# Optimization experiments

Measured on AMD Instinct MI355X. Metric: run time of the kernel, lower is better.

The kernel has to match this reference:

```python
import jax, jax.numpy as jnp
import numpy as np
import itertools

N_PARTICLES = 8388608
GRID_RES = 2048
BOX_SIZE = 1000.0

def _rotations_47():
    perms = list(itertools.permutations([0, 1, 2]))
    signs = list(itertools.product([1, -1], repeat=3))
    mats = []
    for s in signs:
        for p in perms:
            M = np.zeros((3, 3), np.float32)
            M[0, p[0]] = s[0]; M[1, p[1]] = s[1]; M[2, p[2]] = s[2]
            mats.append(M)
    return jnp.asarray(np.stack(mats)[1:])  # drop identity -> 47 matrices

# Analytic stand-ins for jax_cosmo background quantities (EdS-like forms).
def _Gp(a):
    return a ** 1.5

def _dGfa(a):
    return 1.5 * jnp.sqrt(a)

def _a_of_chi(chi):
    return 1.0 / (1.0 + chi / 3000.0)

def _paint_2d(pos, center, width, box_size, res):
    """CIC scatter of particles inside a z-slab onto a [res,res] density plane."""
    z = pos[:, 2]
    sel = ((z >= center - width * 0.5) & (z < center + width * 0.5)).astype(pos.dtype)
    xy = pos[:, :2] * (res / box_size)          # grid coordinates, [N,2]
    i0 = jnp.floor(xy)
    f = xy - i0                                  # CIC fractional offsets
    i0 = i0.astype(jnp.int32)
    ix0 = jnp.mod(i0[:, 0], res); iy0 = jnp.mod(i0[:, 1], res)
    ix1 = jnp.mod(i0[:, 0] + 1, res); iy1 = jnp.mod(i0[:, 1] + 1, res)
    fx, fy = f[:, 0], f[:, 1]
    flat = jnp.zeros((res * res,), dtype=pos.dtype)
    flat = flat.at[ix0 * res + iy0].add(sel * (1 - fx) * (1 - fy))
    flat = flat.at[ix1 * res + iy0].add(sel * fx * (1 - fy))
    flat = flat.at[ix0 * res + iy1].add(sel * (1 - fx) * fy)
    flat = flat.at[ix1 * res + iy1].add(sel * fx * fy)
    return flat.reshape(res, res)

def setup_inputs():
    key = jax.random.key(0)
    k1, k2 = jax.random.split(key)
    positions = jax.random.uniform(k1, (N_PARTICLES, 3), jnp.float32) * BOX_SIZE
    velocities = jax.random.normal(k2, (N_PARTICLES, 3), jnp.float32) * 2.0
    return {
        "positions": positions,
        "velocities": velocities,
        "rotations": _rotations_47(),
        "observer": jnp.zeros((3,), jnp.float32),
        "r_centers": jnp.asarray([250.0, 750.0, 1250.0, 1750.0], jnp.float32),
        "density_widths": jnp.full((4,), 500.0, jnp.float32),
        "t": jnp.float32(0.8),
        "max_comoving_distance": jnp.float32(BOX_SIZE),
        "box_size": jnp.float32(BOX_SIZE),
        "shell_idx": 2,
        "rotation_idx": 1,
        "grid_res": GRID_RES,
    }

def reference(positions, velocities, rotations, observer, r_centers, density_widths,
              t, max_comoving_distance, box_size, shell_idx, rotation_idx, grid_res):
    r_center = r_centers[shell_idx]
    width = density_widths[shell_idx]
    inside_box = r_center + width * 0.5 <= max_comoving_distance

    def inside_branch(args):
        pos, _vel = args
        return _paint_2d(pos, r_center, width, box_size, grid_res)

    def telephoto_branch(args):
        pos, vel = args
        M = rotations[rotation_idx % 47]                                   # [3,3]
        shift = jnp.floor(r_center / max_comoving_distance) * max_comoving_distance
        p_rot = (pos - observer) @ M.T                                      # rotate about observer
        z_axis = jnp.array([0.0, 0.0, 1.0], pos.dtype)
        p_shift = p_rot + z_axis * shift
        v_rot = vel @ M.T
        dist = jnp.linalg.norm(p_shift - observer, axis=-1)                 # [N]
        a_tgt = _a_of_chi(dist)[:, None]                                    # per-particle target scale factor
        ac = jnp.sqrt(t * a_tgt)
        drift = (_Gp(a_tgt) - _Gp(t)) / _dGfa(ac)
        p_drift = p_shift + drift * v_rot
        return _paint_2d(p_drift + observer, r_center, width, box_size, grid_res)

    return jax.lax.cond(inside_box, inside_branch, telephoto_branch, (positions, velocities))
```

## Files before the change

kernel.cpp:

```cpp
#include <hip/hip_runtime.h>
#include <cmath>


#define TSZ    128
#define NBKT   256
#define CAPB   2
#define SLOTS  (CAPB*16)
#define DEPTH  26
#define NTH    256
#define NBLK   960
#define VEC    4
#define NSUB   3
#define DESCMAX 256
#define SENT   0xFFFFFFFFu

__device__ __forceinline__ float fast_rcp(float x)  { return __builtin_amdgcn_rcpf(x); }
__device__ __forceinline__ float fast_sqrt(float x) { return __builtin_amdgcn_sqrtf(x); }

__device__ __forceinline__ int wrap_idx(int v, int res) {
    v += (v < 0) ? res : 0;
    v += (v < 0) ? res : 0;
    v += (v < 0) ? res : 0;
    v -= (v >= res) ? res : 0;
    v -= (v >= res) ? res : 0;
    v -= (v >= res) ? res : 0;
    if (v < 0 || v >= res) { v %= res; if (v < 0) v += res; }
    return v;
}

__device__ __forceinline__ void scatter_direct(float* __restrict__ out, int res,
                                               int gx0, int gy0, float fx, float fy) {
    int gx1 = gx0 + 1; if (gx1 >= res) gx1 = 0;
    int gy1 = gy0 + 1; if (gy1 >= res) gy1 = 0;
    atomicAdd(&out[gx0 * res + gy0], (1.0f - fx) * (1.0f - fy));
    atomicAdd(&out[gx1 * res + gy0], fx * (1.0f - fy));
    atomicAdd(&out[gx0 * res + gy1], (1.0f - fx) * fy);
    atomicAdd(&out[gx1 * res + gy1], fx * fy);
}

__device__ __forceinline__ void rec_decode(unsigned rec, int b, int tiles,
                                           int& gx, int& gy, float& fx, float& fy) {
    int tx = b / tiles, ty = b - tx * tiles;
    gx = (tx << 7) + (int)(rec >> 25);
    gy = (ty << 7) + (int)((rec >> 18) & 127u);
    fx = (float)((rec >> 9) & 511u) * (1.0f / 512.0f);
    fy = (float)(rec & 511u) * (1.0f / 512.0f);
}

struct Uni {
    float m00, m01, m02, m10, m11, m12, m20, m21, m22;
    float ox, oy, oz, shift;
    float r_lo, r_hi, t, gp_t, scale;
    int   resm1, res, tiles;
    bool  inside;
};

struct PR {
    unsigned rec, st;
    int ix0, iy0;
    float fx, fy;
    bool val;
};

__device__ __forceinline__ PR tp_compute(
    const Uni& u, unsigned dummy,
    float px, float py, float pz, float vx, float vy, float vz)
{
    float X, Y, Z;
    if (u.inside) {
        X = px; Y = py; Z = pz;
    } else {
        const float qx_ = px - u.ox, qy_ = py - u.oy, qz_ = pz - u.oz;
        float rx = u.m00 * qx_ + u.m01 * qy_ + u.m02 * qz_;
        float ry = u.m10 * qx_ + u.m11 * qy_ + u.m12 * qz_;
        float rz = u.m20 * qx_ + u.m21 * qy_ + u.m22 * qz_ + u.shift;

        const float vrx = u.m00 * vx + u.m01 * vy + u.m02 * vz;
        const float vry = u.m10 * vx + u.m11 * vy + u.m12 * vz;
        const float vrz = u.m20 * vx + u.m21 * vy + u.m22 * vz;

        const float dx = rx - u.ox, dy = ry - u.oy, dz = rz - u.oz;
        const float dist  = fast_sqrt(dx * dx + dy * dy + dz * dz);
        const float a_tgt = fast_rcp(1.0f + dist * (1.0f / 3000.0f));
        const float ac    = fast_sqrt(u.t * a_tgt);
        const float gp_a  = a_tgt * fast_sqrt(a_tgt);
        const float drift = (gp_a - u.gp_t) * fast_rcp(1.5f * fast_sqrt(ac));

        X = rx + drift * vrx + u.ox;
        Y = ry + drift * vry + u.oy;
        Z = rz + drift * vrz + u.oz;
    }
    PR o;
    o.val = (Z >= u.r_lo && Z < u.r_hi);

    const float gx = X * u.scale, gy = Y * u.scale;
    const float fgx = floorf(gx), fgy = floorf(gy);
    o.fx = gx - fgx; o.fy = gy - fgy;
    o.ix0 = ((int)fgx) & u.resm1;
    o.iy0 = ((int)fgy) & u.resm1;
    const unsigned st = (unsigned)((o.ix0 >> 7) * u.tiles + (o.iy0 >> 7));
    o.st = o.val ? st : dummy;

    unsigned qx = (unsigned)(o.fx * 512.0f + 0.5f); if (qx > 511u) qx = 511u;
    unsigned qy = (unsigned)(o.fy * 512.0f + 0.5f); if (qy > 511u) qy = 511u;
    o.rec = ((unsigned)(o.ix0 & 127) << 25) | ((unsigned)(o.iy0 & 127) << 18)
          | (qx << 9) | qy;
    return o;
}

__device__ __forceinline__ void tp_finish(
    const Uni& u, const PR& o, unsigned p,
    unsigned* __restrict__ fill, unsigned* __restrict__ buf,
    float* __restrict__ out)
{
    if (!o.val) return;
    if (p < DEPTH) buf[o.st * DEPTH + p] = o.rec;
    else { atomicSub(&fill[o.st], 1u); scatter_direct(out, u.res, o.ix0, o.iy0, o.fx, o.fy); }
}

__device__ __forceinline__ void tp_process(
    const Uni& u, float px, float py, float pz, float vx, float vy, float vz,
    unsigned* __restrict__ fill, unsigned* __restrict__ buf,
    float* __restrict__ out)
{
    const PR o = tp_compute(u, 0u, px, py, pz, vx, vy, vz);
    if (!o.val) return;
    unsigned p = atomicAdd(&fill[o.st], 1u);
    tp_finish(u, o, p, fill, buf, out);
}

__global__ __launch_bounds__(NTH) void tp_bin(
    const float* __restrict__ pos, const float* __restrict__ vel,
    const float* __restrict__ rotations, const float* __restrict__ observer,
    const float* __restrict__ r_centers, const float* __restrict__ widths,
    const float* __restrict__ t_p, const float* __restrict__ maxd_p,
    const float* __restrict__ box_p, const int* __restrict__ shell_p,
    const int* __restrict__ ridx_p,
    unsigned char* __restrict__ cnts, unsigned* __restrict__ grec,
    float* __restrict__ out, int res, int tiles, int n, int rounds)
{
    __shared__ unsigned fill[NBKT + 64];
    __shared__ unsigned buf[NBKT * DEPTH];
    __shared__ unsigned descB[DESCMAX];
    __shared__ unsigned descD[DESCMAX];
    __shared__ unsigned char cidA[NBKT];
    __shared__ unsigned ndesc;

    const int tid = threadIdx.x;
    for (int b = tid; b < NBKT + 64; b += NTH) fill[b] = 0;
    if (tid < NBKT) cidA[tid] = 0;
    if (tid == 0) ndesc = 0;

    Uni u;
    {
        const int   shell    = shell_p[0];
        const float r_center = r_centers[shell];
        const float width    = widths[shell];
        const float maxd     = maxd_p[0];
        const float box      = box_p[0];
        u.t      = t_p[0];
        u.inside = (r_center + width * 0.5f) <= maxd;
        int ridx = ridx_p[0] % 47; if (ridx < 0) ridx += 47;
        const float* M = rotations + 9 * ridx;
        u.m00 = M[0]; u.m01 = M[1]; u.m02 = M[2];
        u.m10 = M[3]; u.m11 = M[4]; u.m12 = M[5];
        u.m20 = M[6]; u.m21 = M[7]; u.m22 = M[8];
        u.ox = observer[0]; u.oy = observer[1]; u.oz = observer[2];
        u.shift = floorf(r_center / maxd) * maxd;
        u.r_lo = r_center - width * 0.5f;
        u.r_hi = r_center + width * 0.5f;
        u.gp_t = u.t * sqrtf(u.t);
        u.scale = (float)res / box;
        u.resm1 = res - 1; u.res = res; u.tiles = tiles;
    }

    const unsigned dummy = (unsigned)(NBKT + (tid & 63));
    const float4* __restrict__ pos4 = (const float4*)pos;
    const float4* __restrict__ vel4 = (const float4*)vel;

    __syncthreads();

    for (int r = 0; r < rounds; ++r) {
        #pragma unroll 1
        for (int s = 0; s < NSUB; ++s) {
            const int rc = r * NSUB + s;
            const int base = ((rc * NBLK + blockIdx.x) * NTH + tid) * VEC;
            if (base + VEC <= n) {
                const int q = base * 3 / 4;
                const float4 a = pos4[q], b = pos4[q + 1], c = pos4[q + 2];
                PR r0, r1, r2, r3;
                if (u.inside) {
                    r0 = tp_compute(u, dummy, a.x, a.y, a.z, 0, 0, 0);
                    r1 = tp_compute(u, dummy, a.w, b.x, b.y, 0, 0, 0);
                    r2 = tp_compute(u, dummy, b.z, b.w, c.x, 0, 0, 0);
                    r3 = tp_compute(u, dummy, c.y, c.z, c.w, 0, 0, 0);
                } else {
                    const float4 d = vel4[q], e = vel4[q + 1], f = vel4[q + 2];
                    r0 = tp_compute(u, dummy, a.x, a.y, a.z, d.x, d.y, d.z);
                    r1 = tp_compute(u, dummy, a.w, b.x, b.y, d.w, e.x, e.y);
                    r2 = tp_compute(u, dummy, b.z, b.w, c.x, e.z, e.w, f.x);
                    r3 = tp_compute(u, dummy, c.y, c.z, c.w, f.y, f.z, f.w);
                }
                const unsigned p0 = atomicAdd(&fill[r0.st], 1u);
                const unsigned p1 = atomicAdd(&fill[r1.st], 1u);
                const unsigned p2 = atomicAdd(&fill[r2.st], 1u);
                const unsigned p3 = atomicAdd(&fill[r3.st], 1u);
                tp_finish(u, r0, p0, fill, buf, out);
                tp_finish(u, r1, p1, fill, buf, out);
                tp_finish(u, r2, p2, fill, buf, out);
                tp_finish(u, r3, p3, fill, buf, out);
            } else {
                for (int p = 0; p < VEC; ++p) {
                    const int i = base + p;
                    if (i >= 0 && i < n)
                        tp_process(u, pos[3 * i], pos[3 * i + 1], pos[3 * i + 2],
                                   vel[3 * i], vel[3 * i + 1], vel[3 * i + 2],
                                   fill, buf, out);
                }
            }
        }
        __syncthreads();
        if (tid < NBKT) {
            const unsigned c = fill[tid];
            const unsigned k = c >> 4;
            if (k) {
                unsigned d = atomicAdd(&ndesc, k);
                unsigned cid = cidA[tid];
                for (unsigned g = 0; g < k; ++g) {
                    descB[d + g] = (unsigned)tid | ((g * 16u) << 16);
                    descD[d + g] = (cid < CAPB)
                        ? (unsigned)(((unsigned)tid * NBLK + blockIdx.x) * SLOTS + cid * 16u)
                        : SENT;
                    ++cid;
                }
                cidA[tid] = (unsigned char)cid;
            }
        }
        __syncthreads();
        const unsigned nd = ndesc;
        for (unsigned did = (unsigned)(tid >> 4); did < nd; did += NTH / 16) {
            const unsigned e = descB[did];
            const unsigned b = e & 0xffffu, so = e >> 16;
            const unsigned rv = buf[b * DEPTH + so + (tid & 15)];
            const unsigned dstb = descD[did];
            if (dstb != SENT) {
                grec[(size_t)dstb + (tid & 15)] = rv;
            } else {
                int gx0, gy0; float ffx, ffy;
                rec_decode(rv, (int)b, u.tiles, gx0, gy0, ffx, ffy);
                scatter_direct(out, u.res, gx0, gy0, ffx, ffy);
            }
        }
        __syncthreads();
        if (tid < NBKT) {
            const unsigned c = fill[tid];
            const unsigned k = c >> 4;
            if (k) {
                const unsigned resid = c - 16u * k;
                for (unsigned j = 0; j < resid; ++j)
                    buf[tid * DEPTH + j] = buf[tid * DEPTH + 16u * k + j];
                fill[tid] = resid;
            }
        }
        if (tid == 0) ndesc = 0;
        __syncthreads();
    }

    if (tid < NBKT) {
        const unsigned c = fill[tid];
        const unsigned cid = cidA[tid];
        const unsigned wc = (cid < CAPB) ? cid : (unsigned)CAPB;
        const bool rw = (c > 0) && (cid < CAPB);
        cnts[(size_t)blockIdx.x * NBKT + tid] = (unsigned char)(16u * wc + (rw ? c : 0u));
        if (c) {
            unsigned d = atomicAdd(&ndesc, 1u);
            descB[d] = (unsigned)tid | (c << 16);
            descD[d] = rw
                ? (unsigned)(((unsigned)tid * NBLK + blockIdx.x) * SLOTS + cid * 16u)
                : SENT;
        }
    }
    __syncthreads();
    const unsigned nd = ndesc;
    for (unsigned did = (unsigned)(tid >> 4); did < nd; did += NTH / 16) {
        const unsigned e = descB[did];
        const unsigned b = e & 0xffffu, c = e >> 16;
        const unsigned lane = (unsigned)(tid & 15);
        if (lane < c) {
            const unsigned rv = buf[b * DEPTH + lane];
            const unsigned dstb = descD[did];
            if (dstb != SENT) {
                grec[(size_t)dstb + lane] = rv;
            } else {
                int gx0, gy0; float ffx, ffy;
                rec_decode(rv, (int)b, u.tiles, gx0, gy0, ffx, ffy);
                scatter_direct(out, u.res, gx0, gy0, ffx, ffy);
            }
        }
    }
}

__global__ __launch_bounds__(1024) void tp_paint(
    const unsigned char* __restrict__ cnts, const unsigned* __restrict__ grec,
    float* __restrict__ out, int res, int tiles)
{
    __shared__ unsigned long long quad[4][64 * 64];
    __shared__ unsigned char cs[NBLK];
    const int b = blockIdx.x;
    const int tx = b / tiles, ty = b - tx * tiles;

    for (int c = threadIdx.x; c < 4 * 64 * 64; c += blockDim.x)
        quad[c >> 12][c & 4095] = 0ull;
    for (int i = threadIdx.x; i < NBLK; i += blockDim.x)
        cs[i] = cnts[(size_t)i * NBKT + b];
    __syncthreads();

    const unsigned* __restrict__ rr = grec + (size_t)b * NBLK * SLOTS;
    const int total = NBLK * SLOTS;
    for (int idx = threadIdx.x; idx < total; idx += blockDim.x) {
        const unsigned p = rr[idx];
        if ((idx & (SLOTS - 1)) < (int)cs[idx >> 5]) {
            const int li = (int)(p >> 25);
            const int lj = (int)((p >> 18) & 127u);
            const unsigned qx = (p >> 9) & 511u;
            const unsigned qy = p & 511u;
            const unsigned ax = 512u - qx, ay = 512u - qy;
            const unsigned long long w00 = (ax * ay + 128u) >> 8;
            const unsigned long long w01 = (ax * qy + 128u) >> 8;
            const unsigned long long w10 = (qx * ay + 128u) >> 8;
            const unsigned long long w11 = (qx * qy + 128u) >> 8;
            const unsigned long long pk = w00 | (w01 << 16) | (w10 << 32) | (w11 << 48);
            const int g = ((li & 1) << 1) | (lj & 1);
            atomicAdd(&quad[g][(li >> 1) * 64 + (lj >> 1)], pk);
        }
    }
    __syncthreads();

    for (int c = threadIdx.x; c < (TSZ + 1) * (TSZ + 1); c += blockDim.x) {
        const int i = c / (TSZ + 1), j = c - i * (TSZ + 1);
        unsigned acc = 0;
        #pragma unroll
        for (int r = 0; r < 2; ++r) {
            const int ii = i - r;
            if (ii < 0 || ii > TSZ - 1) continue;
            #pragma unroll
            for (int s = 0; s < 2; ++s) {
                const int jj = j - s;
                if (jj < 0 || jj > TSZ - 1) continue;
                const int g = ((ii & 1) << 1) | (jj & 1);
                const unsigned long long v = quad[g][(ii >> 1) * 64 + (jj >> 1)];
                acc += (unsigned)((v >> (16 * (r * 2 + s))) & 0xffffull);
            }
        }
        const float val = (float)acc * (1.0f / 1024.0f);
        int gx = tx * TSZ + i; if (gx >= res) gx -= res;
        int gy = ty * TSZ + j; if (gy >= res) gy -= res;
        float* dst = &out[gx * res + gy];
        if (i == 0 || j == 0 || i == TSZ || j == TSZ) {
            if (val != 0.0f) atomicAdd(dst, val);
        } else {
            *dst += val;
        }
    }
}

__global__ __launch_bounds__(256) void tp_direct(
    const float* __restrict__ pos, const float* __restrict__ vel,
    const float* __restrict__ rotations, const float* __restrict__ observer,
    const float* __restrict__ r_centers, const float* __restrict__ widths,
    const float* __restrict__ t_p, const float* __restrict__ maxd_p,
    const float* __restrict__ box_p, const int* __restrict__ shell_p,
    const int* __restrict__ ridx_p, float* __restrict__ out, int res, int n)
{
    int i = blockIdx.x * blockDim.x + threadIdx.x;
    if (i >= n) return;
    const int   shell    = shell_p[0];
    const float r_center = r_centers[shell];
    const float width    = widths[shell];
    const float maxd     = maxd_p[0];
    const float box      = box_p[0];
    const float t        = t_p[0];
    const bool  inside   = (r_center + width * 0.5f) <= maxd;
    int ridx = ridx_p[0] % 47; if (ridx < 0) ridx += 47;

    float px = pos[3 * i], py = pos[3 * i + 1], pz = pos[3 * i + 2];
    float X, Y, Z;
    if (inside) {
        X = px; Y = py; Z = pz;
    } else {
        const float* M = rotations + 9 * ridx;
        const float ox = observer[0], oy = observer[1], oz = observer[2];
        const float qx = px - ox, qy = py - oy, qz = pz - oz;
        float rx = M[0] * qx + M[1] * qy + M[2] * qz;
        float ry = M[3] * qx + M[4] * qy + M[5] * qz;
        float rz = M[6] * qx + M[7] * qy + M[8] * qz + floorf(r_center / maxd) * maxd;
        const float vx = vel[3 * i], vy = vel[3 * i + 1], vz = vel[3 * i + 2];
        const float vrx = M[0] * vx + M[1] * vy + M[2] * vz;
        const float vry = M[3] * vx + M[4] * vy + M[5] * vz;
        const float vrz = M[6] * vx + M[7] * vy + M[8] * vz;
        const float dx = rx - ox, dy = ry - oy, dz = rz - oz;
        const float dist  = sqrtf(dx * dx + dy * dy + dz * dz);
        const float a_tgt = 1.0f / (1.0f + dist / 3000.0f);
        const float ac    = sqrtf(t * a_tgt);
        const float drift = (a_tgt * sqrtf(a_tgt) - t * sqrtf(t)) / (1.5f * sqrtf(ac));
        X = rx + drift * vrx + ox;
        Y = ry + drift * vry + oy;
        Z = rz + drift * vrz + oz;
    }
    if (!(Z >= r_center - width * 0.5f && Z < r_center + width * 0.5f)) return;

    const float scale = (float)res / box;
    const float gx = X * scale, gy = Y * scale;
    const float fgx = floorf(gx), fgy = floorf(gy);
    scatter_direct(out, res, wrap_idx((int)fgx, res), wrap_idx((int)fgy, res),
                   gx - fgx, gy - fgy);
}

extern "C" void kernel_launch(void* const* d_in, const int* in_sizes, int n_in,
                              void* d_out, int out_size, void* d_ws, size_t ws_size,
                              hipStream_t stream) {
    const float* pos   = (const float*)d_in[0];
    const float* velv  = (const float*)d_in[1];
    const float* rot   = (const float*)d_in[2];
    const float* obs   = (const float*)d_in[3];
    const float* rc    = (const float*)d_in[4];
    const float* dw    = (const float*)d_in[5];
    const float* t     = (const float*)d_in[6];
    const float* maxd  = (const float*)d_in[7];
    const float* box   = (const float*)d_in[8];
    const int*   shell = (const int*)d_in[9];
    const int*   ridx  = (const int*)d_in[10];
    float* out = (float*)d_out;

    const int n   = in_sizes[0] / 3;
    const int res = (int)llround(sqrt((double)out_size));

    hipMemsetAsync(out, 0, (size_t)out_size * sizeof(float), stream);

    const int tiles = res / TSZ;
    const int nt2 = tiles * tiles;
    const size_t rec_bytes = (size_t)NBKT * NBLK * SLOTS * sizeof(unsigned);
    const size_t cnt_bytes = (size_t)NBLK * NBKT;
    const bool pow2 = res > 0 && (res & (res - 1)) == 0;

    if (!pow2 || res % TSZ != 0 || nt2 > NBKT ||
        (long long)res * res != (long long)out_size ||
        ws_size < rec_bytes + cnt_bytes) {
        tp_direct<<<(n + 255) / 256, 256, 0, stream>>>(
            pos, velv, rot, obs, rc, dw, t, maxd, box, shell, ridx, out, res, n);
        return;
    }

    unsigned* grec = (unsigned*)d_ws;
    unsigned char* cnts = (unsigned char*)d_ws + rec_bytes;

    const int per_round = NBLK * NTH * VEC * NSUB;
    const int rounds = (n + per_round - 1) / per_round;
    tp_bin<<<NBLK, NTH, 0, stream>>>(
        pos, velv, rot, obs, rc, dw, t, maxd, box, shell, ridx,
        cnts, grec, out, res, tiles, n, rounds);

    tp_paint<<<nt2, 1024, 0, stream>>>(cnts, grec, out, res, tiles);
}
```

Before: 295.3 us.

## Make binning wave-private with eager per-bucket flushes instead of block-wide rounds

The binning kernel now gives each wavefront its own shared-memory fill counters, bucket buffers and chunk ids. When a bucket reaches 16 records, the lane that took slot 15 flushes it at once, instead of the block running barrier-separated rounds with a descriptor list. This removes the __syncthreads and descriptor bookkeeping per round. The cost is that a single lane flushes each bucket serially with copies and residual shifts, each wave gets only one global chunk per bucket before falling back to direct atomic scatter, and the paint kernel now scans a record array indexed per wave.

Result: faster. 289.2 us (-2.1%).

```diff
diff --git a/kernel.cpp b/kernel.cpp
--- a/kernel.cpp
+++ b/kernel.cpp
@@ -4,15 +4,13 @@
 
 #define TSZ    128
 #define NBKT   256
-#define CAPB   2
-#define SLOTS  (CAPB*16)
-#define DEPTH  26
+#define DEPTH  18
+#define SLOTS  16
 #define NTH    256
-#define NBLK   960
+#define WPB    4
+#define NBLK   480
+#define NWAVES (NBLK*WPB)
 #define VEC    4
-#define NSUB   3
-#define DESCMAX 256
-#define SENT   0xFFFFFFFFu
 
 __device__ __forceinline__ float fast_rcp(float x)  { return __builtin_amdgcn_rcpf(x); }
 __device__ __forceinline__ float fast_sqrt(float x) { return __builtin_amdgcn_sqrtf(x); }
@@ -118,15 +116,40 @@
     else { atomicSub(&fill[o.st], 1u); scatter_direct(out, u.res, o.ix0, o.iy0, o.fx, o.fy); }
 }
 
-__device__ __forceinline__ void tp_process(
-    const Uni& u, float px, float py, float pz, float vx, float vy, float vz,
+__device__ __forceinline__ void flush_if(
+    const Uni& u, const PR& o, unsigned p, unsigned w,
     unsigned* __restrict__ fill, unsigned* __restrict__ buf,
-    float* __restrict__ out)
-{
-    const PR o = tp_compute(u, 0u, px, py, pz, vx, vy, vz);
-    if (!o.val) return;
-    unsigned p = atomicAdd(&fill[o.st], 1u);
-    tp_finish(u, o, p, fill, buf, out);
+    unsigned char* __restrict__ cid,
+    unsigned* __restrict__ grec, float* __restrict__ out)
+{
+    if (o.val && p == 15u) {
+        const unsigned b = o.st;
+        const unsigned c = fill[b];
+        const unsigned ci = cid[b];
+        if (ci == 0u) {
+            const size_t dst = ((size_t)b * NWAVES + w) * SLOTS;
+            #pragma unroll
+            for (int i = 0; i < 16; i += 4) {
+                uint4 v;
+                v.x = buf[b * DEPTH + i];
+                v.y = buf[b * DEPTH + i + 1];
+                v.z = buf[b * DEPTH + i + 2];
+                v.w = buf[b * DEPTH + i + 3];
+                *(uint4*)(grec + dst + i) = v;
+            }
+        } else {
+            for (int i = 0; i < 16; ++i) {
+                int gx0, gy0; float ffx, ffy;
+                rec_decode(buf[b * DEPTH + i], (int)b, u.tiles, gx0, gy0, ffx, ffy);
+                scatter_direct(out, u.res, gx0, gy0, ffx, ffy);
+            }
+        }
+        cid[b] = (unsigned char)(ci + 1u);
+        const unsigned resid = c - 16u;
+        for (unsigned j = 0; j < resid; ++j)
+            buf[b * DEPTH + j] = buf[b * DEPTH + 16u + j];
+        fill[b] = resid;
+    }
 }
 
 __global__ __launch_bounds__(NTH) void tp_bin(
@@ -137,19 +160,21 @@
     const float* __restrict__ box_p, const int* __restrict__ shell_p,
     const int* __restrict__ ridx_p,
     unsigned char* __restrict__ cnts, unsigned* __restrict__ grec,
-    float* __restrict__ out, int res, int tiles, int n, int rounds)
-{
-    __shared__ unsigned fill[NBKT + 64];
-    __shared__ unsigned buf[NBKT * DEPTH];
-    __shared__ unsigned descB[DESCMAX];
-    __shared__ unsigned descD[DESCMAX];
-    __shared__ unsigned char cidA[NBKT];
-    __shared__ unsigned ndesc;
-
-    const int tid = threadIdx.x;
-    for (int b = tid; b < NBKT + 64; b += NTH) fill[b] = 0;
-    if (tid < NBKT) cidA[tid] = 0;
-    if (tid == 0) ndesc = 0;
+    float* __restrict__ out, int res, int tiles, int n, int cpw)
+{
+    __shared__ unsigned fillS[WPB][NBKT + 64];
+    __shared__ unsigned bufS[WPB][NBKT * DEPTH];
+    __shared__ unsigned char cidS[WPB][NBKT];
+
+    const int tid  = threadIdx.x;
+    const int wv   = tid >> 6;
+    const int lane = tid & 63;
+    unsigned* __restrict__ fill = fillS[wv];
+    unsigned* __restrict__ buf  = bufS[wv];
+    unsigned char* __restrict__ cid = cidS[wv];
+
+    for (int b = lane; b < NBKT + 64; b += 64) fill[b] = 0;
+    for (int b = lane; b < NBKT; b += 64) cid[b] = 0;
 
     Uni u;
     {
@@ -174,129 +199,74 @@
         u.resm1 = res - 1; u.res = res; u.tiles = tiles;
     }
 
-    const unsigned dummy = (unsigned)(NBKT + (tid & 63));
+    const unsigned w = (unsigned)(blockIdx.x * WPB + wv);
+    const unsigned dummy = (unsigned)(NBKT + lane);
     const float4* __restrict__ pos4 = (const float4*)pos;
     const float4* __restrict__ vel4 = (const float4*)vel;
 
-    __syncthreads();
-
-    for (int r = 0; r < rounds; ++r) {
-        #pragma unroll 1
-        for (int s = 0; s < NSUB; ++s) {
-            const int rc = r * NSUB + s;
-            const int base = ((rc * NBLK + blockIdx.x) * NTH + tid) * VEC;
-            if (base + VEC <= n) {
-                const int q = base * 3 / 4;
-                const float4 a = pos4[q], b = pos4[q + 1], c = pos4[q + 2];
-                PR r0, r1, r2, r3;
-                if (u.inside) {
-                    r0 = tp_compute(u, dummy, a.x, a.y, a.z, 0, 0, 0);
-                    r1 = tp_compute(u, dummy, a.w, b.x, b.y, 0, 0, 0);
-                    r2 = tp_compute(u, dummy, b.z, b.w, c.x, 0, 0, 0);
-                    r3 = tp_compute(u, dummy, c.y, c.z, c.w, 0, 0, 0);
-                } else {
-                    const float4 d = vel4[q], e = vel4[q + 1], f = vel4[q + 2];
-                    r0 = tp_compute(u, dummy, a.x, a.y, a.z, d.x, d.y, d.z);
-                    r1 = tp_compute(u, dummy, a.w, b.x, b.y, d.w, e.x, e.y);
-                    r2 = tp_compute(u, dummy, b.z, b.w, c.x, e.z, e.w, f.x);
-                    r3 = tp_compute(u, dummy, c.y, c.z, c.w, f.y, f.z, f.w);
+    for (int k = 0; k < cpw; ++k) {
+        const int base = (((k * NWAVES + (int)w) * 64) + lane) * VEC;
+        PR pr[4];
+        if (base + VEC <= n) {
+            const int q = base * 3 / 4;
+            const float4 a = pos4[q], b = pos4[q + 1], c = pos4[q + 2];
+            if (u.inside) {
+                pr[0] = tp_compute(u, dummy, a.x, a.y, a.z, 0, 0, 0);
+                pr[1] = tp_compute(u, dummy, a.w, b.x, b.y, 0, 0, 0);
+                pr[2] = tp_compute(u, dummy, b.z, b.w, c.x, 0, 0, 0);
+                pr[3] = tp_compute(u, dummy, c.y, c.z, c.w, 0, 0, 0);
+            } else {
+                const float4 d = vel4[q], e = vel4[q + 1], f = vel4[q + 2];
+                pr[0] = tp_compute(u, dummy, a.x, a.y, a.z, d.x, d.y, d.z);
+                pr[1] = tp_compute(u, dummy, a.w, b.x, b.y, d.w, e.x, e.y);
+                pr[2] = tp_compute(u, dummy, b.z, b.w, c.x, e.z, e.w, f.x);
+                pr[3] = tp_compute(u, dummy, c.y, c.z, c.w, f.y, f.z, f.w);
+            }
+        } else {
+            #pragma unroll
+            for (int j = 0; j < VEC; ++j) {
+                const int i = base + j;
+                const bool ok = (i >= 0) && (i < n);
+                float px = 0, py = 0, pz = 0, vx = 0, vy = 0, vz = 0;
+                if (ok) {
+                    px = pos[3 * i]; py = pos[3 * i + 1]; pz = pos[3 * i + 2];
+                    if (!u.inside) {
+                        vx = vel[3 * i]; vy = vel[3 * i + 1]; vz = vel[3 * i + 2];
+                    }
                 }
-                const unsigned p0 = atomicAdd(&fill[r0.st], 1u);
-                const unsigned p1 = atomicAdd(&fill[r1.st], 1u);
-                const unsigned p2 = atomicAdd(&fill[r2.st], 1u);
-                const unsigned p3 = atomicAdd(&fill[r3.st], 1u);
-                tp_finish(u, r0, p0, fill, buf, out);
-                tp_finish(u, r1, p1, fill, buf, out);
-                tp_finish(u, r2, p2, fill, buf, out);
-                tp_finish(u, r3, p3, fill, buf, out);
-            } else {
-                for (int p = 0; p < VEC; ++p) {
-                    const int i = base + p;
-                    if (i >= 0 && i < n)
-                        tp_process(u, pos[3 * i], pos[3 * i + 1], pos[3 * i + 2],
-                                   vel[3 * i], vel[3 * i + 1], vel[3 * i + 2],
-                                   fill, buf, out);
-                }
-            }
-        }
-        __syncthreads();
-        if (tid < NBKT) {
-            const unsigned c = fill[tid];
-            const unsigned k = c >> 4;
-            if (k) {
-                unsigned d = atomicAdd(&ndesc, k);
-                unsigned cid = cidA[tid];
-                for (unsigned g = 0; g < k; ++g) {
-                    descB[d + g] = (unsigned)tid | ((g * 16u) << 16);
-                    descD[d + g] = (cid < CAPB)
-                        ? (unsigned)(((unsigned)tid * NBLK + blockIdx.x) * SLOTS + cid * 16u)
-                        : SENT;
-                    ++cid;
-                }
-                cidA[tid] = (unsigned char)cid;
-            }
-        }
-        __syncthreads();
-        const unsigned nd = ndesc;
-        for (unsigned did = (unsigned)(tid >> 4); did < nd; did += NTH / 16) {
-            const unsigned e = descB[did];
-            const unsigned b = e & 0xffffu, so = e >> 16;
-            const unsigned rv = buf[b * DEPTH + so + (tid & 15)];
-            const unsigned dstb = descD[did];
-            if (dstb != SENT) {
-                grec[(size_t)dstb + (tid & 15)] = rv;
-            } else {
+                PR t = tp_compute(u, dummy, px, py, pz, vx, vy, vz);
+                if (!ok) { t.val = false; t.st = dummy; }
+                pr[j] = t;
+            }
+        }
+        unsigned pp[4];
+        #pragma unroll
+        for (int j = 0; j < 4; ++j) pp[j] = atomicAdd(&fill[pr[j].st], 1u);
+        #pragma unroll
+        for (int j = 0; j < 4; ++j) tp_finish(u, pr[j], pp[j], fill, buf, out);
+        #pragma unroll
+        for (int j = 0; j < 4; ++j) flush_if(u, pr[j], pp[j], w, fill, buf, cid, grec, out);
+    }
+
+    #pragma unroll
+    for (int j = 0; j < NBKT / 64; ++j) {
+        const int b = lane + j * 64;
+        const unsigned c = fill[b];
+        const unsigned ci = cid[b];
+        unsigned char cb;
+        if (ci == 0u) {
+            cb = (unsigned char)c;
+            const size_t dst = ((size_t)b * NWAVES + w) * SLOTS;
+            for (unsigned i = 0; i < c; ++i) grec[dst + i] = buf[b * DEPTH + i];
+        } else {
+            cb = (unsigned char)SLOTS;
+            for (unsigned i = 0; i < c; ++i) {
                 int gx0, gy0; float ffx, ffy;
-                rec_decode(rv, (int)b, u.tiles, gx0, gy0, ffx, ffy);
+                rec_decode(buf[b * DEPTH + i], b, u.tiles, gx0, gy0, ffx, ffy);
                 scatter_direct(out, u.res, gx0, gy0, ffx, ffy);
             }
         }
-        __syncthreads();
-        if (tid < NBKT) {
-            const unsigned c = fill[tid];
-            const unsigned k = c >> 4;
-            if (k) {
-                const unsigned resid = c - 16u * k;
-                for (unsigned j = 0; j < resid; ++j)
-                    buf[tid * DEPTH + j] = buf[tid * DEPTH + 16u * k + j];
-                fill[tid] = resid;
-            }
-        }
-        if (tid == 0) ndesc = 0;
-        __syncthreads();
-    }
-
-    if (tid < NBKT) {
-        const unsigned c = fill[tid];
-        const unsigned cid = cidA[tid];
-        const unsigned wc = (cid < CAPB) ? cid : (unsigned)CAPB;
-        const bool rw = (c > 0) && (cid < CAPB);
-        cnts[(size_t)blockIdx.x * NBKT + tid] = (unsigned char)(16u * wc + (rw ? c : 0u));
-        if (c) {
-            unsigned d = atomicAdd(&ndesc, 1u);
-            descB[d] = (unsigned)tid | (c << 16);
-            descD[d] = rw
-                ? (unsigned)(((unsigned)tid * NBLK + blockIdx.x) * SLOTS + cid * 16u)
-                : SENT;
-        }
-    }
-    __syncthreads();
-    const unsigned nd = ndesc;
-    for (unsigned did = (unsigned)(tid >> 4); did < nd; did += NTH / 16) {
-        const unsigned e = descB[did];
-        const unsigned b = e & 0xffffu, c = e >> 16;
-        const unsigned lane = (unsigned)(tid & 15);
-        if (lane < c) {
-            const unsigned rv = buf[b * DEPTH + lane];
-            const unsigned dstb = descD[did];
-            if (dstb != SENT) {
-                grec[(size_t)dstb + lane] = rv;
-            } else {
-                int gx0, gy0; float ffx, ffy;
-                rec_decode(rv, (int)b, u.tiles, gx0, gy0, ffx, ffy);
-                scatter_direct(out, u.res, gx0, gy0, ffx, ffy);
-            }
-        }
+        cnts[(size_t)w * NBKT + b] = cb;
     }
 }
 
@@ -305,21 +275,21 @@
     float* __restrict__ out, int res, int tiles)
 {
     __shared__ unsigned long long quad[4][64 * 64];
-    __shared__ unsigned char cs[NBLK];
+    __shared__ unsigned char cs[NWAVES];
     const int b = blockIdx.x;
     const int tx = b / tiles, ty = b - tx * tiles;
 
     for (int c = threadIdx.x; c < 4 * 64 * 64; c += blockDim.x)
         quad[c >> 12][c & 4095] = 0ull;
-    for (int i = threadIdx.x; i < NBLK; i += blockDim.x)
+    for (int i = threadIdx.x; i < NWAVES; i += blockDim.x)
         cs[i] = cnts[(size_t)i * NBKT + b];
     __syncthreads();
 
-    const unsigned* __restrict__ rr = grec + (size_t)b * NBLK * SLOTS;
-    const int total = NBLK * SLOTS;
+    const unsigned* __restrict__ rr = grec + (size_t)b * NWAVES * SLOTS;
+    const int total = NWAVES * SLOTS;
     for (int idx = threadIdx.x; idx < total; idx += blockDim.x) {
         const unsigned p = rr[idx];
-        if ((idx & (SLOTS - 1)) < (int)cs[idx >> 5]) {
+        if ((idx & (SLOTS - 1)) < (int)cs[idx >> 4]) {
             const int li = (int)(p >> 25);
             const int lj = (int)((p >> 18) & 127u);
             const unsigned qx = (p >> 9) & 511u;
@@ -439,8 +409,8 @@
 
     const int tiles = res / TSZ;
     const int nt2 = tiles * tiles;
-    const size_t rec_bytes = (size_t)NBKT * NBLK * SLOTS * sizeof(unsigned);
-    const size_t cnt_bytes = (size_t)NBLK * NBKT;
+    const size_t rec_bytes = (size_t)NBKT * NWAVES * SLOTS * sizeof(unsigned);
+    const size_t cnt_bytes = (size_t)NWAVES * NBKT;
     const bool pow2 = res > 0 && (res & (res - 1)) == 0;
 
     if (!pow2 || res % TSZ != 0 || nt2 > NBKT ||
@@ -454,11 +424,11 @@
     unsigned* grec = (unsigned*)d_ws;
     unsigned char* cnts = (unsigned char*)d_ws + rec_bytes;
 
-    const int per_round = NBLK * NTH * VEC * NSUB;
-    const int rounds = (n + per_round - 1) / per_round;
+    const int per_sweep = NWAVES * 64 * VEC;
+    const int cpw = (n + per_sweep - 1) / per_sweep;
     tp_bin<<<NBLK, NTH, 0, stream>>>(
         pos, velv, rot, obs, rc, dw, t, maxd, box, shell, ridx,
-        cnts, grec, out, res, tiles, n, rounds);
+        cnts, grec, out, res, tiles, n, cpw);
 
     tp_paint<<<nt2, 1024, 0, stream>>>(cnts, grec, out, res, tiles);
 }
```
